# Optimization experiments

Measured on AMD Instinct MI355X. Metric: run time of the kernel, lower is better.

Reference implementation:

```python
import jax, jax.numpy as jnp
import numpy as np

NUM_HEAD = 16
HEAD_DIM = 64
SEQ, BATCH, DMODEL = 2048, 2, 1024


def setup_inputs() -> dict:
    key = jax.random.key(0)
    ks = jax.random.split(key, 6)
    xavier = lambda k, shp: jax.random.uniform(
        k, shp, jnp.float32, -1.0, 1.0) * np.sqrt(6.0 / (shp[0] + shp[1]))
    query = jax.random.normal(ks[0], (SEQ, BATCH, DMODEL), jnp.float32)
    q_w = xavier(ks[1], (DMODEL, DMODEL))
    k_w = xavier(ks[2], (DMODEL, DMODEL))
    v_w = xavier(ks[3], (DMODEL, DMODEL))
    out_w = xavier(ks[4], (DMODEL, DMODEL))
    zeros = jnp.zeros((DMODEL,), jnp.float32)
    # causal mask: True = masked out (key position after query position)
    causal = jnp.triu(jnp.ones((SEQ, SEQ), bool), k=1)
    attn_mask = jnp.broadcast_to(causal, (BATCH, SEQ, SEQ))
    return {
        "query": query,
        "q_w": q_w, "q_b": zeros,
        "k_w": k_w, "k_b": zeros,
        "v_w": v_w, "v_b": zeros,
        "out_w": out_w, "out_b": zeros,
        "attn_mask": attn_mask,
    }


def reference(query, q_w, q_b, k_w, k_b, v_w, v_b, out_w, out_b, attn_mask):
    S, B, _ = query.shape
    H, Dh = NUM_HEAD, HEAD_DIM
    scale = 1.0 / np.sqrt(Dh)
    # self-attention: key = value = query
    q = (query @ q_w.T + q_b).reshape(S, B, H, Dh)
    k = (query @ k_w.T + k_b).reshape(S, B, H, Dh)
    v = (query @ v_w.T + v_b).reshape(S, B, H, Dh)
    # scores: [B, H, S(query), S(key)]
    scores = jnp.einsum('sbhd,tbhd->bhst', q, k) * scale
    scores = jnp.where(attn_mask[:, None, :, :], -jnp.inf, scores)
    attn = jax.nn.softmax(scores, axis=-1)
    # context: [S, B, H, Dh] -> [S, B, H*Dh]
    ctx = jnp.einsum('bhst,tbhd->sbhd', attn, v).reshape(S, B, H * Dh)
    return ctx @ out_w.T + out_b
```

## Files before the change

kernel.cpp:

```cpp
#include <hip/hip_runtime.h>
#include <hip/hip_bf16.h>

typedef __bf16 bf16;
typedef __attribute__((ext_vector_type(2))) __bf16 bf16x2;
typedef __attribute__((ext_vector_type(4))) __bf16 bf16x4;
typedef __attribute__((ext_vector_type(8))) __bf16 bf16x8;
typedef __attribute__((ext_vector_type(4))) float f32x4;

static_assert(sizeof(bf16x8) == 16, "bf16x8 must be 16B");

#define S_LEN 2048
#define BATCH_N 2
#define DM 1024
#define NHEAD 16
#define HDIM 64
#define LOG2E 1.44269504088896f

__device__ __forceinline__ void async_cp16(const void* g, void* l) {
    __builtin_amdgcn_global_load_lds(
        (const __attribute__((address_space(1))) void*)g,
        (__attribute__((address_space(3))) void*)l, 16, 0, 0);
}

__global__ __launch_bounds__(256)
void cvt_all(const float* __restrict__ q,
             const float* __restrict__ w0, const float* __restrict__ w1,
             const float* __restrict__ w2, const float* __restrict__ w3,
             bf16* __restrict__ Xb,
             bf16* __restrict__ W0, bf16* __restrict__ W1,
             bf16* __restrict__ W2, bf16* __restrict__ W3) {
    const int blk = blockIdx.x;
    const float* src;
    bf16* dst;
    size_t base;
    if (blk < 2048) {
        src = q; dst = Xb; base = (size_t)blk * 2048;
    } else {
        const int w = (blk - 2048) >> 9;
        const int r = (blk - 2048) & 511;
        base = (size_t)r * 2048;
        src = (w == 0) ? w0 : (w == 1) ? w1 : (w == 2) ? w2 : w3;
        dst = (w == 0) ? W0 : (w == 1) ? W1 : (w == 2) ? W2 : W3;
    }
    const size_t i = base + (size_t)threadIdx.x * 8;
    const f32x4 a = *(const f32x4*)(src + i);
    const f32x4 b = *(const f32x4*)(src + i + 4);
    bf16x8 r8;
    r8[0] = (bf16)a[0]; r8[1] = (bf16)a[1]; r8[2] = (bf16)a[2]; r8[3] = (bf16)a[3];
    r8[4] = (bf16)b[0]; r8[5] = (bf16)b[1]; r8[6] = (bf16)b[2]; r8[7] = (bf16)b[3];
    *(bf16x8*)(dst + i) = r8;
}

__device__ __forceinline__ void gemm_tile(const bf16* __restrict__ A,
                                          const bf16* __restrict__ W,
                                          int row0, int col0, int Kdim,
                                          f32x4 acc[4][4]) {
    __shared__ bf16 As[128 * 32];
    __shared__ bf16 Bs[128 * 32];
    const int tid  = threadIdx.x;
    const int lane = tid & 63;
    const int wv   = tid >> 6;
    const int wr = wv >> 1, wc = wv & 1;
    const int qr = lane & 15, quad = lane >> 4;

    const int srow = wv * 16 + (lane >> 2);
    const int scol = (lane & 3) * 8;
    const bf16* Ap = A + (size_t)(row0 + srow) * Kdim + scol;
    const bf16* Wp = W + (size_t)(col0 + srow) * Kdim + scol;
    bf16* lA0 = As + wv * 512;
    bf16* lA1 = As + 64 * 32 + wv * 512;
    bf16* lB0 = Bs + wv * 512;
    bf16* lB1 = Bs + 64 * 32 + wv * 512;

    const f32x4 fzero = {0.f, 0.f, 0.f, 0.f};
    #pragma unroll
    for (int mi = 0; mi < 4; ++mi)
        #pragma unroll
        for (int ni = 0; ni < 4; ++ni)
            acc[mi][ni] = fzero;

    for (int k0 = 0; k0 < Kdim; k0 += 32) {
        __syncthreads();
        async_cp16(Ap + k0, lA0);
        async_cp16(Ap + (size_t)64 * Kdim + k0, lA1);
        async_cp16(Wp + k0, lB0);
        async_cp16(Wp + (size_t)64 * Kdim + k0, lB1);
        __syncthreads();

        bf16x8 af[4], bfr[4];
        #pragma unroll
        for (int mi = 0; mi < 4; ++mi)
            af[mi] = *(const bf16x8*)(As + (wr * 64 + mi * 16 + qr) * 32 + quad * 8);
        #pragma unroll
        for (int ni = 0; ni < 4; ++ni)
            bfr[ni] = *(const bf16x8*)(Bs + (wc * 64 + ni * 16 + qr) * 32 + quad * 8);
        #pragma unroll
        for (int mi = 0; mi < 4; ++mi)
            #pragma unroll
            for (int ni = 0; ni < 4; ++ni)
                acc[mi][ni] = __builtin_amdgcn_mfma_f32_16x16x32_bf16(
                    af[mi], bfr[ni], acc[mi][ni], 0, 0, 0);
    }
}

__global__ __launch_bounds__(256)
void qkv_kernel(const bf16* __restrict__ X,
                const bf16* __restrict__ Wq, const float* __restrict__ bq,
                const bf16* __restrict__ Wk, const float* __restrict__ bk,
                const bf16* __restrict__ Wv, const float* __restrict__ bv,
                bf16* __restrict__ Q, bf16* __restrict__ Kt, bf16* __restrict__ Vt) {
    const int mat  = blockIdx.z;
    const bf16*  W    = (mat == 0) ? Wq : (mat == 1) ? Wk : Wv;
    const float* bias = (mat == 0) ? bq : (mat == 1) ? bk : bv;
    const int col0 = blockIdx.x * 128;
    const int row0 = blockIdx.y * 128;

    f32x4 acc[4][4];
    gemm_tile(X, W, row0, col0, DM, acc);

    const int lane = threadIdx.x & 63;
    const int wave = threadIdx.x >> 6;
    const int wr = wave >> 1, wc = wave & 1;
    const int qr = lane & 15, quad = lane >> 4;

    #pragma unroll
    for (int ni = 0; ni < 4; ++ni) {
        const int n  = col0 + wc * 64 + ni * 16 + qr;
        const float bn = bias[n];
        const int h = n >> 6, dh = n & 63;
        #pragma unroll
        for (int mi = 0; mi < 4; ++mi) {
            const int i0 = row0 + wr * 64 + mi * 16 + quad * 4;
            const float v0 = acc[mi][ni][0] + bn;
            const float v1 = acc[mi][ni][1] + bn;
            const float v2 = acc[mi][ni][2] + bn;
            const float v3 = acc[mi][ni][3] + bn;
            if (mat == 2) {
                const int s0 = i0 >> 1;
                bf16x2 e0 = {(bf16)v0, (bf16)v2};
                bf16x2 e1 = {(bf16)v1, (bf16)v3};
                *(bf16x2*)(Vt + ((size_t)h * HDIM + dh) * S_LEN + s0) = e0;
                *(bf16x2*)(Vt + ((size_t)(NHEAD + h) * HDIM + dh) * S_LEN + s0) = e1;
            } else {
                #pragma unroll
                for (int r = 0; r < 4; ++r) {
                    const int i = i0 + r;
                    const int s = i >> 1, b = i & 1;
                    const float v = (r == 0) ? v0 : (r == 1) ? v1 : (r == 2) ? v2 : v3;
                    if (mat == 0) {
                        Q[((size_t)(b * NHEAD + h) * S_LEN + s) * HDIM + dh] =
                            (bf16)(v * (0.125f * LOG2E));
                    } else {
                        Kt[((size_t)(b * NHEAD + h) * S_LEN + s) * HDIM + dh] = (bf16)v;
                    }
                }
            }
        }
    }
}

#define PLD 40
#define PT  640
#define RSTRIDE 36

#define MFMA(a, b, c) __builtin_amdgcn_mfma_f32_16x16x32_bf16(a, b, c, 0, 0, 0)
#define EX(x) __builtin_amdgcn_exp2f(x)

#define QK_TILE(j) \
    f32x4 sA##j = MFMA(k0, qlo##j, fzero); sA##j = MFMA(k1, qhi##j, sA##j); \
    f32x4 sB##j = MFMA(k2, qlo##j, fzero); sB##j = MFMA(k3, qhi##j, sB##j);

#define SFULL(j) do { \
    const float e0 = EX(sA##j[0]), e1 = EX(sA##j[1]), e2 = EX(sA##j[2]), e3 = EX(sA##j[3]); \
    const float f0 = EX(sB##j[0]), f1 = EX(sB##j[1]), f2 = EX(sB##j[2]), f3 = EX(sB##j[3]); \
    l##j += (e0 + e1 + e2 + e3) + (f0 + f1 + f2 + f3); \
    bf16x4 wa = {(bf16)e0, (bf16)e1, (bf16)e2, (bf16)e3}; \
    bf16x4 wb = {(bf16)f0, (bf16)f1, (bf16)f2, (bf16)f3}; \
    *(bf16x4*)(Pw + (j) * PT + qr * PLD + quad * 4)      = wa; \
    *(bf16x4*)(Pw + (j) * PT + qr * PLD + 16 + quad * 4) = wb; \
} while (0)

#define SMASK(j) do { \
    const int qrow = qb0 + 16 * (j) + qr; \
    const int ka = t * 32 + quad * 4; \
    const float e0 = (ka + 0  <= qrow) ? EX(sA##j[0]) : 0.f; \
    const float e1 = (ka + 1  <= qrow) ? EX(sA##j[1]) : 0.f; \
    const float e2 = (ka + 2  <= qrow) ? EX(sA##j[2]) : 0.f; \
    const float e3 = (ka + 3  <= qrow) ? EX(sA##j[3]) : 0.f; \
    const float f0 = (ka + 16 <= qrow) ? EX(sB##j[0]) : 0.f; \
    const float f1 = (ka + 17 <= qrow) ? EX(sB##j[1]) : 0.f; \
    const float f2 = (ka + 18 <= qrow) ? EX(sB##j[2]) : 0.f; \
    const float f3 = (ka + 19 <= qrow) ? EX(sB##j[3]) : 0.f; \
    l##j += (e0 + e1 + e2 + e3) + (f0 + f1 + f2 + f3); \
    bf16x4 wa = {(bf16)e0, (bf16)e1, (bf16)e2, (bf16)e3}; \
    bf16x4 wb = {(bf16)f0, (bf16)f1, (bf16)f2, (bf16)f3}; \
    *(bf16x4*)(Pw + (j) * PT + qr * PLD + quad * 4)      = wa; \
    *(bf16x4*)(Pw + (j) * PT + qr * PLD + 16 + quad * 4) = wb; \
} while (0)

__global__ __launch_bounds__(256)
void attn_part(const bf16* __restrict__ Q, const bf16* __restrict__ K,
               const bf16* __restrict__ Vt,
               bf16* __restrict__ Pout, float* __restrict__ Pl) {
    __shared__ __align__(16) char smem[27648];
    const int lane = threadIdx.x & 63;
    const int wave = threadIdx.x >> 6;
    const int qr = lane & 15, quad = lane >> 4;
    const int bh = blockIdx.y;
    const int f  = blockIdx.x;
    int qb, c;
    if (f < 8)       { qb = f;                c = 0; }
    else if (f < 24) { qb = 8 + ((f - 8) >> 1);  c = (f - 8) & 1; }
    else if (f < 48) { qb = 16 + (f - 24) / 3;   c = (f - 24) % 3; }
    else             { qb = 24 + ((f - 48) >> 2); c = (f - 48) & 3; }
    const int qb0    = qb * 64;
    const int tdiag  = qb * 2;
    const int ntiles = 2 * qb + 2;
    const int t0     = c * 16;
    const int tend   = min(t0 + 16, ntiles);

    const bf16* Qb = Q  + (size_t)bh * S_LEN * HDIM;
    const bf16* Kb = K  + (size_t)bh * S_LEN * HDIM;
    const bf16* Vb = Vt + (size_t)bh * HDIM * S_LEN;

    const bf16x8 qlo0 = *(const bf16x8*)(Qb + (size_t)(qb0 + qr) * HDIM + quad * 8);
    const bf16x8 qhi0 = *(const bf16x8*)(Qb + (size_t)(qb0 + qr) * HDIM + quad * 8 + 32);
    const bf16x8 qlo1 = *(const bf16x8*)(Qb + (size_t)(qb0 + 16 + qr) * HDIM + quad * 8);
    const bf16x8 qhi1 = *(const bf16x8*)(Qb + (size_t)(qb0 + 16 + qr) * HDIM + quad * 8 + 32);
    const bf16x8 qlo2 = *(const bf16x8*)(Qb + (size_t)(qb0 + 32 + qr) * HDIM + quad * 8);
    const bf16x8 qhi2 = *(const bf16x8*)(Qb + (size_t)(qb0 + 32 + qr) * HDIM + quad * 8 + 32);
    const bf16x8 qlo3 = *(const bf16x8*)(Qb + (size_t)(qb0 + 48 + qr) * HDIM + quad * 8);
    const bf16x8 qhi3 = *(const bf16x8*)(Qb + (size_t)(qb0 + 48 + qr) * HDIM + quad * 8 + 32);

    const f32x4 fzero = {0.f, 0.f, 0.f, 0.f};
    f32x4 o0_0 = fzero, o0_1 = fzero, o0_2 = fzero, o0_3 = fzero;
    f32x4 o1_0 = fzero, o1_1 = fzero, o1_2 = fzero, o1_3 = fzero;
    f32x4 o2_0 = fzero, o2_1 = fzero, o2_2 = fzero, o2_3 = fzero;
    f32x4 o3_0 = fzero, o3_1 = fzero, o3_2 = fzero, o3_3 = fzero;
    float l0 = 0.f, l1 = 0.f, l2 = 0.f, l3 = 0.f;
    bf16* Pw = (bf16*)smem + wave * (4 * PT);

    for (int t = t0 + wave; t < tend; t += 4) {
        const bf16* kp = Kb + ((size_t)t * 32 + qr) * HDIM + quad * 8;
        const bf16x8 k0 = *(const bf16x8*)(kp);
        const bf16x8 k1 = *(const bf16x8*)(kp + 32);
        const bf16x8 k2 = *(const bf16x8*)(kp + 16 * HDIM);
        const bf16x8 k3 = *(const bf16x8*)(kp + 16 * HDIM + 32);
        const bf16* vp = Vb + (size_t)qr * S_LEN + t * 32 + quad * 8;
        const bf16x8 v0 = *(const bf16x8*)(vp);
        const bf16x8 v1 = *(const bf16x8*)(vp + 16 * S_LEN);
        const bf16x8 v2 = *(const bf16x8*)(vp + 32 * S_LEN);
        const bf16x8 v3 = *(const bf16x8*)(vp + 48 * S_LEN);

        if (t < tdiag) {
            QK_TILE(0); SFULL(0);
            QK_TILE(1); SFULL(1);
            QK_TILE(2); SFULL(2);
            QK_TILE(3); SFULL(3);
        } else {
            QK_TILE(0); SMASK(0);
            QK_TILE(1); SMASK(1);
            QK_TILE(2); SMASK(2);
            QK_TILE(3); SMASK(3);
        }

        const bf16x8 pf0 = *(const bf16x8*)(Pw + 0 * PT + qr * PLD + quad * 8);
        const bf16x8 pf1 = *(const bf16x8*)(Pw + 1 * PT + qr * PLD + quad * 8);
        const bf16x8 pf2 = *(const bf16x8*)(Pw + 2 * PT + qr * PLD + quad * 8);
        const bf16x8 pf3 = *(const bf16x8*)(Pw + 3 * PT + qr * PLD + quad * 8);
        o0_0 = MFMA(v0, pf0, o0_0); o0_1 = MFMA(v1, pf0, o0_1);
        o0_2 = MFMA(v2, pf0, o0_2); o0_3 = MFMA(v3, pf0, o0_3);
        o1_0 = MFMA(v0, pf1, o1_0); o1_1 = MFMA(v1, pf1, o1_1);
        o1_2 = MFMA(v2, pf1, o1_2); o1_3 = MFMA(v3, pf1, o1_3);
        o2_0 = MFMA(v0, pf2, o2_0); o2_1 = MFMA(v1, pf2, o2_1);
        o2_2 = MFMA(v2, pf2, o2_2); o2_3 = MFMA(v3, pf2, o2_3);
        o3_0 = MFMA(v0, pf3, o3_0); o3_1 = MFMA(v1, pf3, o3_1);
        o3_2 = MFMA(v2, pf3, o3_2); o3_3 = MFMA(v3, pf3, o3_3);
    }

    __syncthreads();
    float* red = (float*)smem;
    if (wave != 0) {
        float* rp = red + ((size_t)(wave - 1) * 64 + lane) * RSTRIDE;
        *(f32x4*)(rp +  0) = o0_0; *(f32x4*)(rp +  4) = o0_1;
        *(f32x4*)(rp +  8) = o0_2; *(f32x4*)(rp + 12) = o0_3;
        *(f32x4*)(rp + 16) = o1_0; *(f32x4*)(rp + 20) = o1_1;
        *(f32x4*)(rp + 24) = o1_2; *(f32x4*)(rp + 28) = o1_3;
        rp[32] = l0; rp[33] = l1;
    }
    __syncthreads();
    if (wave == 0) {
        #pragma unroll
        for (int w = 0; w < 3; ++w) {
            const float* rp = red + ((size_t)w * 64 + lane) * RSTRIDE;
            o0_0 += *(const f32x4*)(rp +  0); o0_1 += *(const f32x4*)(rp +  4);
            o0_2 += *(const f32x4*)(rp +  8); o0_3 += *(const f32x4*)(rp + 12);
            o1_0 += *(const f32x4*)(rp + 16); o1_1 += *(const f32x4*)(rp + 20);
            o1_2 += *(const f32x4*)(rp + 24); o1_3 += *(const f32x4*)(rp + 28);
            l0 += rp[32]; l1 += rp[33];
        }
    }
    __syncthreads();
    if (wave != 0) {
        float* rp = red + ((size_t)(wave - 1) * 64 + lane) * RSTRIDE;
        *(f32x4*)(rp +  0) = o2_0; *(f32x4*)(rp +  4) = o2_1;
        *(f32x4*)(rp +  8) = o2_2; *(f32x4*)(rp + 12) = o2_3;
        *(f32x4*)(rp + 16) = o3_0; *(f32x4*)(rp + 20) = o3_1;
        *(f32x4*)(rp + 24) = o3_2; *(f32x4*)(rp + 28) = o3_3;
        rp[32] = l2; rp[33] = l3;
    }
    __syncthreads();
    if (wave == 0) {
        #pragma unroll
        for (int w = 0; w < 3; ++w) {
            const float* rp = red + ((size_t)w * 64 + lane) * RSTRIDE;
            o2_0 += *(const f32x4*)(rp +  0); o2_1 += *(const f32x4*)(rp +  4);
            o2_2 += *(const f32x4*)(rp +  8); o2_3 += *(const f32x4*)(rp + 12);
            o3_0 += *(const f32x4*)(rp + 16); o3_1 += *(const f32x4*)(rp + 20);
            o3_2 += *(const f32x4*)(rp + 24); o3_3 += *(const f32x4*)(rp + 28);
            l2 += rp[32]; l3 += rp[33];
        }
        l0 += __shfl_xor(l0, 16); l0 += __shfl_xor(l0, 32);
        l1 += __shfl_xor(l1, 16); l1 += __shfl_xor(l1, 32);
        l2 += __shfl_xor(l2, 16); l2 += __shfl_xor(l2, 32);
        l3 += __shfl_xor(l3, 16); l3 += __shfl_xor(l3, 32);

        const size_t sidx = ((size_t)bh * 32 + qb) * 4 + c;
        bf16* po = Pout + sidx * 4096;
        float* pl = Pl + sidx * 64;
        #define PWRITE(ov, ni_, jrow_) do { \
            bf16x4 cc = {(bf16)ov[0], (bf16)ov[1], (bf16)ov[2], (bf16)ov[3]}; \
            *(bf16x4*)(po + (size_t)((jrow_) * 16 + qr) * 64 + (ni_) * 16 + quad * 4) = cc; \
        } while (0)
        PWRITE(o0_0, 0, 0); PWRITE(o0_1, 1, 0); PWRITE(o0_2, 2, 0); PWRITE(o0_3, 3, 0);
        PWRITE(o1_0, 0, 1); PWRITE(o1_1, 1, 1); PWRITE(o1_2, 2, 1); PWRITE(o1_3, 3, 1);
        PWRITE(o2_0, 0, 2); PWRITE(o2_1, 1, 2); PWRITE(o2_2, 2, 2); PWRITE(o2_3, 3, 2);
        PWRITE(o3_0, 0, 3); PWRITE(o3_1, 1, 3); PWRITE(o3_2, 2, 3); PWRITE(o3_3, 3, 3);
        #undef PWRITE
        if (quad == 0) {
            pl[qr]      = l0;
            pl[16 + qr] = l1;
            pl[32 + qr] = l2;
            pl[48 + qr] = l3;
        }
    }
}

__global__ __launch_bounds__(256)
void attn_reduce(const bf16* __restrict__ Pout, const float* __restrict__ Pl,
                 bf16* __restrict__ ctx) {
    const int qb = blockIdx.x, bh = blockIdx.y;
    const int b = bh >> 4, h = bh & 15;
    const int nc = (qb < 8) ? 1 : (qb < 16) ? 2 : (qb < 24) ? 3 : 4;
    const int tid = threadIdx.x;
    const int row = tid >> 2;
    const int dg  = (tid & 3) * 16;
    const size_t base = ((size_t)bh * 32 + qb) * 4;

    float acc[16];
    #pragma unroll
    for (int i = 0; i < 16; ++i) acc[i] = 0.f;
    float lsum = 0.f;
    for (int cc = 0; cc < nc; ++cc) {
        const bf16* po = Pout + (base + cc) * 4096 + (size_t)row * 64 + dg;
        const bf16x8 x0 = *(const bf16x8*)(po);
        const bf16x8 x1 = *(const bf16x8*)(po + 8);
        #pragma unroll
        for (int i = 0; i < 8; ++i) { acc[i] += (float)x0[i]; acc[8 + i] += (float)x1[i]; }
        lsum += Pl[(base + cc) * 64 + row];
    }
    const float inv = 1.f / lsum;
    bf16x8 y0, y1;
    #pragma unroll
    for (int i = 0; i < 8; ++i) { y0[i] = (bf16)(acc[i] * inv); y1[i] = (bf16)(acc[8 + i] * inv); }
    bf16* cp = ctx + ((size_t)(qb * 64 + row) * BATCH_N + b) * DM + h * 64 + dg;
    *(bf16x8*)cp = y0;
    *(bf16x8*)(cp + 8) = y1;
}

__global__ __launch_bounds__(256)
void proj_kernel(const bf16* __restrict__ X, const bf16* __restrict__ W,
                 const float* __restrict__ bias, float* __restrict__ out) {
    const int col0 = blockIdx.x * 128;
    const int row0 = blockIdx.y * 128;
    f32x4 acc[4][4];
    gemm_tile(X, W, row0, col0, DM, acc);

    const int lane = threadIdx.x & 63;
    const int wave = threadIdx.x >> 6;
    const int wr = wave >> 1, wc = wave & 1;
    const int qr = lane & 15, quad = lane >> 4;

    #pragma unroll
    for (int ni = 0; ni < 4; ++ni) {
        const int n = col0 + wc * 64 + ni * 16 + qr;
        const float bn = bias[n];
        #pragma unroll
        for (int mi = 0; mi < 4; ++mi) {
            #pragma unroll
            for (int r = 0; r < 4; ++r) {
                const int i = row0 + wr * 64 + mi * 16 + quad * 4 + r;
                out[(size_t)i * DM + n] = acc[mi][ni][r] + bn;
            }
        }
    }
}

extern "C" void kernel_launch(void* const* d_in, const int* in_sizes, int n_in,
                              void* d_out, int out_size, void* d_ws, size_t ws_size,
                              hipStream_t stream) {
    (void)in_sizes; (void)n_in; (void)out_size; (void)ws_size;
    const float* query = (const float*)d_in[0];
    const float* q_w   = (const float*)d_in[1];
    const float* q_b   = (const float*)d_in[2];
    const float* k_w   = (const float*)d_in[3];
    const float* k_b   = (const float*)d_in[4];
    const float* v_w   = (const float*)d_in[5];
    const float* v_b   = (const float*)d_in[6];
    const float* out_w = (const float*)d_in[7];
    const float* out_b = (const float*)d_in[8];

    char* ws = (char*)d_ws;
    bf16*  Qb   = (bf16*)(ws);
    bf16*  Kb   = (bf16*)(ws + ((size_t)8  << 20));
    bf16*  Vt   = (bf16*)(ws + ((size_t)16 << 20));
    bf16*  ctx  = (bf16*)(ws + ((size_t)24 << 20));
    bf16*  Wob  = (bf16*)(ws + ((size_t)32 << 20));
    bf16*  Xb   = (bf16*)(ws + ((size_t)34 << 20));
    bf16*  Wqb  = (bf16*)(ws + ((size_t)42 << 20));
    bf16*  Wkb  = (bf16*)(ws + ((size_t)44 << 20));
    bf16*  Wvb  = (bf16*)(ws + ((size_t)46 << 20));
    bf16*  Pout = (bf16*)(ws + ((size_t)34 << 20));
    float* Pl   = (float*)(ws + ((size_t)66 << 20));
    float* out  = (float*)d_out;

    dim3 blk(256);
    cvt_all<<<dim3(2048 + 4 * 512), blk, 0, stream>>>(
        query, q_w, k_w, v_w, out_w, Xb, Wqb, Wkb, Wvb, Wob);

    qkv_kernel<<<dim3(DM / 128, (S_LEN * BATCH_N) / 128, 3), blk, 0, stream>>>(
        Xb, Wqb, q_b, Wkb, k_b, Wvb, v_b, Qb, Kb, Vt);
    attn_part<<<dim3(80, BATCH_N * NHEAD), blk, 0, stream>>>(Qb, Kb, Vt, Pout, Pl);
    attn_reduce<<<dim3(S_LEN / 64, BATCH_N * NHEAD), blk, 0, stream>>>(Pout, Pl, ctx);
    proj_kernel<<<dim3(DM / 128, (S_LEN * BATCH_N) / 128), blk, 0, stream>>>(
        ctx, Wob, out_b, out);
}
```

Baseline: 232.9 us.

## Fuse attention partial reduce into attn_part with paired causal q-blocks

Each attention block now handles two query blocks, qb and 31-qb, one after the other and covers the full key range for each. It normalizes the output in-kernel and writes ctx directly. This removes the separate attn_reduce kernel and the bf16 partial-output round trip through global memory. The cost is far fewer blocks (512 instead of 2560) with longer serial loops per wave, so there is less parallelism and latency hiding. Shared memory also grows because the P buffer no longer overlaps the reduction area.

```diff
diff --git a/kernel.cpp b/kernel.cpp
--- a/kernel.cpp
+++ b/kernel.cpp
@@ -200,182 +200,145 @@
 
 __global__ __launch_bounds__(256)
 void attn_part(const bf16* __restrict__ Q, const bf16* __restrict__ K,
-               const bf16* __restrict__ Vt,
-               bf16* __restrict__ Pout, float* __restrict__ Pl) {
-    __shared__ __align__(16) char smem[27648];
+               const bf16* __restrict__ Vt, bf16* __restrict__ ctx) {
+    __shared__ __align__(16) char smem[27648 + 20480];
     const int lane = threadIdx.x & 63;
     const int wave = threadIdx.x >> 6;
     const int qr = lane & 15, quad = lane >> 4;
     const int bh = blockIdx.y;
-    const int f  = blockIdx.x;
-    int qb, c;
-    if (f < 8)       { qb = f;                c = 0; }
-    else if (f < 24) { qb = 8 + ((f - 8) >> 1);  c = (f - 8) & 1; }
-    else if (f < 48) { qb = 16 + (f - 24) / 3;   c = (f - 24) % 3; }
-    else             { qb = 24 + ((f - 48) >> 2); c = (f - 48) & 3; }
-    const int qb0    = qb * 64;
-    const int tdiag  = qb * 2;
-    const int ntiles = 2 * qb + 2;
-    const int t0     = c * 16;
-    const int tend   = min(t0 + 16, ntiles);
+    const int b = bh >> 4, h = bh & 15;
 
     const bf16* Qb = Q  + (size_t)bh * S_LEN * HDIM;
     const bf16* Kb = K  + (size_t)bh * S_LEN * HDIM;
     const bf16* Vb = Vt + (size_t)bh * HDIM * S_LEN;
-
-    const bf16x8 qlo0 = *(const bf16x8*)(Qb + (size_t)(qb0 + qr) * HDIM + quad * 8);
-    const bf16x8 qhi0 = *(const bf16x8*)(Qb + (size_t)(qb0 + qr) * HDIM + quad * 8 + 32);
-    const bf16x8 qlo1 = *(const bf16x8*)(Qb + (size_t)(qb0 + 16 + qr) * HDIM + quad * 8);
-    const bf16x8 qhi1 = *(const bf16x8*)(Qb + (size_t)(qb0 + 16 + qr) * HDIM + quad * 8 + 32);
-    const bf16x8 qlo2 = *(const bf16x8*)(Qb + (size_t)(qb0 + 32 + qr) * HDIM + quad * 8);
-    const bf16x8 qhi2 = *(const bf16x8*)(Qb + (size_t)(qb0 + 32 + qr) * HDIM + quad * 8 + 32);
-    const bf16x8 qlo3 = *(const bf16x8*)(Qb + (size_t)(qb0 + 48 + qr) * HDIM + quad * 8);
-    const bf16x8 qhi3 = *(const bf16x8*)(Qb + (size_t)(qb0 + 48 + qr) * HDIM + quad * 8 + 32);
-
+    float* red = (float*)smem;
+    bf16* Pw = (bf16*)(smem + 27648) + wave * (4 * PT);
     const f32x4 fzero = {0.f, 0.f, 0.f, 0.f};
-    f32x4 o0_0 = fzero, o0_1 = fzero, o0_2 = fzero, o0_3 = fzero;
-    f32x4 o1_0 = fzero, o1_1 = fzero, o1_2 = fzero, o1_3 = fzero;
-    f32x4 o2_0 = fzero, o2_1 = fzero, o2_2 = fzero, o2_3 = fzero;
-    f32x4 o3_0 = fzero, o3_1 = fzero, o3_2 = fzero, o3_3 = fzero;
-    float l0 = 0.f, l1 = 0.f, l2 = 0.f, l3 = 0.f;
-    bf16* Pw = (bf16*)smem + wave * (4 * PT);
-
-    for (int t = t0 + wave; t < tend; t += 4) {
-        const bf16* kp = Kb + ((size_t)t * 32 + qr) * HDIM + quad * 8;
-        const bf16x8 k0 = *(const bf16x8*)(kp);
-        const bf16x8 k1 = *(const bf16x8*)(kp + 32);
-        const bf16x8 k2 = *(const bf16x8*)(kp + 16 * HDIM);
-        const bf16x8 k3 = *(const bf16x8*)(kp + 16 * HDIM + 32);
-        const bf16* vp = Vb + (size_t)qr * S_LEN + t * 32 + quad * 8;
-        const bf16x8 v0 = *(const bf16x8*)(vp);
-        const bf16x8 v1 = *(const bf16x8*)(vp + 16 * S_LEN);
-        const bf16x8 v2 = *(const bf16x8*)(vp + 32 * S_LEN);
-        const bf16x8 v3 = *(const bf16x8*)(vp + 48 * S_LEN);
-
-        if (t < tdiag) {
-            QK_TILE(0); SFULL(0);
-            QK_TILE(1); SFULL(1);
-            QK_TILE(2); SFULL(2);
-            QK_TILE(3); SFULL(3);
-        } else {
-            QK_TILE(0); SMASK(0);
-            QK_TILE(1); SMASK(1);
-            QK_TILE(2); SMASK(2);
-            QK_TILE(3); SMASK(3);
-        }
-
-        const bf16x8 pf0 = *(const bf16x8*)(Pw + 0 * PT + qr * PLD + quad * 8);
-        const bf16x8 pf1 = *(const bf16x8*)(Pw + 1 * PT + qr * PLD + quad * 8);
-        const bf16x8 pf2 = *(const bf16x8*)(Pw + 2 * PT + qr * PLD + quad * 8);
-        const bf16x8 pf3 = *(const bf16x8*)(Pw + 3 * PT + qr * PLD + quad * 8);
-        o0_0 = MFMA(v0, pf0, o0_0); o0_1 = MFMA(v1, pf0, o0_1);
-        o0_2 = MFMA(v2, pf0, o0_2); o0_3 = MFMA(v3, pf0, o0_3);
-        o1_0 = MFMA(v0, pf1, o1_0); o1_1 = MFMA(v1, pf1, o1_1);
-        o1_2 = MFMA(v2, pf1, o1_2); o1_3 = MFMA(v3, pf1, o1_3);
-        o2_0 = MFMA(v0, pf2, o2_0); o2_1 = MFMA(v1, pf2, o2_1);
-        o2_2 = MFMA(v2, pf2, o2_2); o2_3 = MFMA(v3, pf2, o2_3);
-        o3_0 = MFMA(v0, pf3, o3_0); o3_1 = MFMA(v1, pf3, o3_1);
-        o3_2 = MFMA(v2, pf3, o3_2); o3_3 = MFMA(v3, pf3, o3_3);
+
+    for (int phase = 0; phase < 2; ++phase) {
+        const int qb = phase ? (31 - (int)blockIdx.x) : (int)blockIdx.x;
+        const int qb0    = qb * 64;
+        const int tdiag  = qb * 2;
+        const int ntiles = 2 * qb + 2;
+
+        const bf16x8 qlo0 = *(const bf16x8*)(Qb + (size_t)(qb0 + qr) * HDIM + quad * 8);
+        const bf16x8 qhi0 = *(const bf16x8*)(Qb + (size_t)(qb0 + qr) * HDIM + quad * 8 + 32);
+        const bf16x8 qlo1 = *(const bf16x8*)(Qb + (size_t)(qb0 + 16 + qr) * HDIM + quad * 8);
+        const bf16x8 qhi1 = *(const bf16x8*)(Qb + (size_t)(qb0 + 16 + qr) * HDIM + quad * 8 + 32);
+        const bf16x8 qlo2 = *(const bf16x8*)(Qb + (size_t)(qb0 + 32 + qr) * HDIM + quad * 8);
+        const bf16x8 qhi2 = *(const bf16x8*)(Qb + (size_t)(qb0 + 32 + qr) * HDIM + quad * 8 + 32);
+        const bf16x8 qlo3 = *(const bf16x8*)(Qb + (size_t)(qb0 + 48 + qr) * HDIM + quad * 8);
+        const bf16x8 qhi3 = *(const bf16x8*)(Qb + (size_t)(qb0 + 48 + qr) * HDIM + quad * 8 + 32);
+
+        f32x4 o0_0 = fzero, o0_1 = fzero, o0_2 = fzero, o0_3 = fzero;
+        f32x4 o1_0 = fzero, o1_1 = fzero, o1_2 = fzero, o1_3 = fzero;
+        f32x4 o2_0 = fzero, o2_1 = fzero, o2_2 = fzero, o2_3 = fzero;
+        f32x4 o3_0 = fzero, o3_1 = fzero, o3_2 = fzero, o3_3 = fzero;
+        float l0 = 0.f, l1 = 0.f, l2 = 0.f, l3 = 0.f;
+
+        for (int t = wave; t < ntiles; t += 4) {
+            const bf16* kp = Kb + ((size_t)t * 32 + qr) * HDIM + quad * 8;
+            const bf16x8 k0 = *(const bf16x8*)(kp);
+            const bf16x8 k1 = *(const bf16x8*)(kp + 32);
+            const bf16x8 k2 = *(const bf16x8*)(kp + 16 * HDIM);
+            const bf16x8 k3 = *(const bf16x8*)(kp + 16 * HDIM + 32);
+            const bf16* vp = Vb + (size_t)qr * S_LEN + t * 32 + quad * 8;
+            const bf16x8 v0 = *(const bf16x8*)(vp);
+            const bf16x8 v1 = *(const bf16x8*)(vp + 16 * S_LEN);
+            const bf16x8 v2 = *(const bf16x8*)(vp + 32 * S_LEN);
+            const bf16x8 v3 = *(const bf16x8*)(vp + 48 * S_LEN);
+
+            if (t < tdiag) {
+                QK_TILE(0); SFULL(0);
+                QK_TILE(1); SFULL(1);
+                QK_TILE(2); SFULL(2);
+                QK_TILE(3); SFULL(3);
+            } else {
+                QK_TILE(0); SMASK(0);
+                QK_TILE(1); SMASK(1);
+                QK_TILE(2); SMASK(2);
+                QK_TILE(3); SMASK(3);
+            }
+
+            const bf16x8 pf0 = *(const bf16x8*)(Pw + 0 * PT + qr * PLD + quad * 8);
+            const bf16x8 pf1 = *(const bf16x8*)(Pw + 1 * PT + qr * PLD + quad * 8);
+            const bf16x8 pf2 = *(const bf16x8*)(Pw + 2 * PT + qr * PLD + quad * 8);
+            const bf16x8 pf3 = *(const bf16x8*)(Pw + 3 * PT + qr * PLD + quad * 8);
+            o0_0 = MFMA(v0, pf0, o0_0); o0_1 = MFMA(v1, pf0, o0_1);
+            o0_2 = MFMA(v2, pf0, o0_2); o0_3 = MFMA(v3, pf0, o0_3);
+            o1_0 = MFMA(v0, pf1, o1_0); o1_1 = MFMA(v1, pf1, o1_1);
+            o1_2 = MFMA(v2, pf1, o1_2); o1_3 = MFMA(v3, pf1, o1_3);
+            o2_0 = MFMA(v0, pf2, o2_0); o2_1 = MFMA(v1, pf2, o2_1);
+            o2_2 = MFMA(v2, pf2, o2_2); o2_3 = MFMA(v3, pf2, o2_3);
+            o3_0 = MFMA(v0, pf3, o3_0); o3_1 = MFMA(v1, pf3, o3_1);
+            o3_2 = MFMA(v2, pf3, o3_2); o3_3 = MFMA(v3, pf3, o3_3);
+        }
+
+        __syncthreads();
+        if (wave != 0) {
+            float* rp = red + ((size_t)(wave - 1) * 64 + lane) * RSTRIDE;
+            *(f32x4*)(rp +  0) = o0_0; *(f32x4*)(rp +  4) = o0_1;
+            *(f32x4*)(rp +  8) = o0_2; *(f32x4*)(rp + 12) = o0_3;
+            *(f32x4*)(rp + 16) = o1_0; *(f32x4*)(rp + 20) = o1_1;
+            *(f32x4*)(rp + 24) = o1_2; *(f32x4*)(rp + 28) = o1_3;
+            rp[32] = l0; rp[33] = l1;
+        }
+        __syncthreads();
+        if (wave == 0) {
+            #pragma unroll
+            for (int w = 0; w < 3; ++w) {
+                const float* rp = red + ((size_t)w * 64 + lane) * RSTRIDE;
+                o0_0 += *(const f32x4*)(rp +  0); o0_1 += *(const f32x4*)(rp +  4);
+                o0_2 += *(const f32x4*)(rp +  8); o0_3 += *(const f32x4*)(rp + 12);
+                o1_0 += *(const f32x4*)(rp + 16); o1_1 += *(const f32x4*)(rp + 20);
+                o1_2 += *(const f32x4*)(rp + 24); o1_3 += *(const f32x4*)(rp + 28);
+                l0 += rp[32]; l1 += rp[33];
+            }
+        }
+        __syncthreads();
+        if (wave != 0) {
+            float* rp = red + ((size_t)(wave - 1) * 64 + lane) * RSTRIDE;
+            *(f32x4*)(rp +  0) = o2_0; *(f32x4*)(rp +  4) = o2_1;
+            *(f32x4*)(rp +  8) = o2_2; *(f32x4*)(rp + 12) = o2_3;
+            *(f32x4*)(rp + 16) = o3_0; *(f32x4*)(rp + 20) = o3_1;
+            *(f32x4*)(rp + 24) = o3_2; *(f32x4*)(rp + 28) = o3_3;
+            rp[32] = l2; rp[33] = l3;
+        }
+        __syncthreads();
+        if (wave == 0) {
+            #pragma unroll
+            for (int w = 0; w < 3; ++w) {
+                const float* rp = red + ((size_t)w * 64 + lane) * RSTRIDE;
+                o2_0 += *(const f32x4*)(rp +  0); o2_1 += *(const f32x4*)(rp +  4);
+                o2_2 += *(const f32x4*)(rp +  8); o2_3 += *(const f32x4*)(rp + 12);
+                o3_0 += *(const f32x4*)(rp + 16); o3_1 += *(const f32x4*)(rp + 20);
+                o3_2 += *(const f32x4*)(rp + 24); o3_3 += *(const f32x4*)(rp + 28);
+                l2 += rp[32]; l3 += rp[33];
+            }
+            l0 += __shfl_xor(l0, 16); l0 += __shfl_xor(l0, 32);
+            l1 += __shfl_xor(l1, 16); l1 += __shfl_xor(l1, 32);
+            l2 += __shfl_xor(l2, 16); l2 += __shfl_xor(l2, 32);
+            l3 += __shfl_xor(l3, 16); l3 += __shfl_xor(l3, 32);
+            const float n0 = 1.f / l0, n1 = 1.f / l1, n2 = 1.f / l2, n3 = 1.f / l3;
+
+            #define CWRITE(ov, ni_, jrow_, nf_) do { \
+                bf16x4 cc = {(bf16)(ov[0] * (nf_)), (bf16)(ov[1] * (nf_)), \
+                             (bf16)(ov[2] * (nf_)), (bf16)(ov[3] * (nf_))}; \
+                const int s_ = qb0 + (jrow_) * 16 + qr; \
+                *(bf16x4*)(ctx + ((size_t)s_ * BATCH_N + b) * DM \
+                           + h * HDIM + (ni_) * 16 + quad * 4) = cc; \
+            } while (0)
+            CWRITE(o0_0, 0, 0, n0); CWRITE(o0_1, 1, 0, n0);
+            CWRITE(o0_2, 2, 0, n0); CWRITE(o0_3, 3, 0, n0);
+            CWRITE(o1_0, 0, 1, n1); CWRITE(o1_1, 1, 1, n1);
+            CWRITE(o1_2, 2, 1, n1); CWRITE(o1_3, 3, 1, n1);
+            CWRITE(o2_0, 0, 2, n2); CWRITE(o2_1, 1, 2, n2);
+            CWRITE(o2_2, 2, 2, n2); CWRITE(o2_3, 3, 2, n2);
+            CWRITE(o3_0, 0, 3, n3); CWRITE(o3_1, 1, 3, n3);
+            CWRITE(o3_2, 2, 3, n3); CWRITE(o3_3, 3, 3, n3);
+            #undef CWRITE
+        }
     }
-
-    __syncthreads();
-    float* red = (float*)smem;
-    if (wave != 0) {
-        float* rp = red + ((size_t)(wave - 1) * 64 + lane) * RSTRIDE;
-        *(f32x4*)(rp +  0) = o0_0; *(f32x4*)(rp +  4) = o0_1;
-        *(f32x4*)(rp +  8) = o0_2; *(f32x4*)(rp + 12) = o0_3;
-        *(f32x4*)(rp + 16) = o1_0; *(f32x4*)(rp + 20) = o1_1;
-        *(f32x4*)(rp + 24) = o1_2; *(f32x4*)(rp + 28) = o1_3;
-        rp[32] = l0; rp[33] = l1;
-    }
-    __syncthreads();
-    if (wave == 0) {
-        #pragma unroll
-        for (int w = 0; w < 3; ++w) {
-            const float* rp = red + ((size_t)w * 64 + lane) * RSTRIDE;
-            o0_0 += *(const f32x4*)(rp +  0); o0_1 += *(const f32x4*)(rp +  4);
-            o0_2 += *(const f32x4*)(rp +  8); o0_3 += *(const f32x4*)(rp + 12);
-            o1_0 += *(const f32x4*)(rp + 16); o1_1 += *(const f32x4*)(rp + 20);
-            o1_2 += *(const f32x4*)(rp + 24); o1_3 += *(const f32x4*)(rp + 28);
-            l0 += rp[32]; l1 += rp[33];
-        }
-    }
-    __syncthreads();
-    if (wave != 0) {
-        float* rp = red + ((size_t)(wave - 1) * 64 + lane) * RSTRIDE;
-        *(f32x4*)(rp +  0) = o2_0; *(f32x4*)(rp +  4) = o2_1;
-        *(f32x4*)(rp +  8) = o2_2; *(f32x4*)(rp + 12) = o2_3;
-        *(f32x4*)(rp + 16) = o3_0; *(f32x4*)(rp + 20) = o3_1;
-        *(f32x4*)(rp + 24) = o3_2; *(f32x4*)(rp + 28) = o3_3;
-        rp[32] = l2; rp[33] = l3;
-    }
-    __syncthreads();
-    if (wave == 0) {
-        #pragma unroll
-        for (int w = 0; w < 3; ++w) {
-            const float* rp = red + ((size_t)w * 64 + lane) * RSTRIDE;
-            o2_0 += *(const f32x4*)(rp +  0); o2_1 += *(const f32x4*)(rp +  4);
-            o2_2 += *(const f32x4*)(rp +  8); o2_3 += *(const f32x4*)(rp + 12);
-            o3_0 += *(const f32x4*)(rp + 16); o3_1 += *(const f32x4*)(rp + 20);
-            o3_2 += *(const f32x4*)(rp + 24); o3_3 += *(const f32x4*)(rp + 28);
-            l2 += rp[32]; l3 += rp[33];
-        }
-        l0 += __shfl_xor(l0, 16); l0 += __shfl_xor(l0, 32);
-        l1 += __shfl_xor(l1, 16); l1 += __shfl_xor(l1, 32);
-        l2 += __shfl_xor(l2, 16); l2 += __shfl_xor(l2, 32);
-        l3 += __shfl_xor(l3, 16); l3 += __shfl_xor(l3, 32);
-
-        const size_t sidx = ((size_t)bh * 32 + qb) * 4 + c;
-        bf16* po = Pout + sidx * 4096;
-        float* pl = Pl + sidx * 64;
-        #define PWRITE(ov, ni_, jrow_) do { \
-            bf16x4 cc = {(bf16)ov[0], (bf16)ov[1], (bf16)ov[2], (bf16)ov[3]}; \
-            *(bf16x4*)(po + (size_t)((jrow_) * 16 + qr) * 64 + (ni_) * 16 + quad * 4) = cc; \
-        } while (0)
-        PWRITE(o0_0, 0, 0); PWRITE(o0_1, 1, 0); PWRITE(o0_2, 2, 0); PWRITE(o0_3, 3, 0);
-        PWRITE(o1_0, 0, 1); PWRITE(o1_1, 1, 1); PWRITE(o1_2, 2, 1); PWRITE(o1_3, 3, 1);
-        PWRITE(o2_0, 0, 2); PWRITE(o2_1, 1, 2); PWRITE(o2_2, 2, 2); PWRITE(o2_3, 3, 2);
-        PWRITE(o3_0, 0, 3); PWRITE(o3_1, 1, 3); PWRITE(o3_2, 2, 3); PWRITE(o3_3, 3, 3);
-        #undef PWRITE
-        if (quad == 0) {
-            pl[qr]      = l0;
-            pl[16 + qr] = l1;
-            pl[32 + qr] = l2;
-            pl[48 + qr] = l3;
-        }
-    }
-}
-
-__global__ __launch_bounds__(256)
-void attn_reduce(const bf16* __restrict__ Pout, const float* __restrict__ Pl,
-                 bf16* __restrict__ ctx) {
-    const int qb = blockIdx.x, bh = blockIdx.y;
-    const int b = bh >> 4, h = bh & 15;
-    const int nc = (qb < 8) ? 1 : (qb < 16) ? 2 : (qb < 24) ? 3 : 4;
-    const int tid = threadIdx.x;
-    const int row = tid >> 2;
-    const int dg  = (tid & 3) * 16;
-    const size_t base = ((size_t)bh * 32 + qb) * 4;
-
-    float acc[16];
-    #pragma unroll
-    for (int i = 0; i < 16; ++i) acc[i] = 0.f;
-    float lsum = 0.f;
-    for (int cc = 0; cc < nc; ++cc) {
-        const bf16* po = Pout + (base + cc) * 4096 + (size_t)row * 64 + dg;
-        const bf16x8 x0 = *(const bf16x8*)(po);
-        const bf16x8 x1 = *(const bf16x8*)(po + 8);
-        #pragma unroll
-        for (int i = 0; i < 8; ++i) { acc[i] += (float)x0[i]; acc[8 + i] += (float)x1[i]; }
-        lsum += Pl[(base + cc) * 64 + row];
-    }
-    const float inv = 1.f / lsum;
-    bf16x8 y0, y1;
-    #pragma unroll
-    for (int i = 0; i < 8; ++i) { y0[i] = (bf16)(acc[i] * inv); y1[i] = (bf16)(acc[8 + i] * inv); }
-    bf16* cp = ctx + ((size_t)(qb * 64 + row) * BATCH_N + b) * DM + h * 64 + dg;
-    *(bf16x8*)cp = y0;
-    *(bf16x8*)(cp + 8) = y1;
 }
 
 __global__ __launch_bounds__(256)
@@ -430,8 +393,6 @@
     bf16*  Wqb  = (bf16*)(ws + ((size_t)42 << 20));
     bf16*  Wkb  = (bf16*)(ws + ((size_t)44 << 20));
     bf16*  Wvb  = (bf16*)(ws + ((size_t)46 << 20));
-    bf16*  Pout = (bf16*)(ws + ((size_t)34 << 20));
-    float* Pl   = (float*)(ws + ((size_t)66 << 20));
     float* out  = (float*)d_out;
 
     dim3 blk(256);
@@ -440,8 +401,7 @@
 
     qkv_kernel<<<dim3(DM / 128, (S_LEN * BATCH_N) / 128, 3), blk, 0, stream>>>(
         Xb, Wqb, q_b, Wkb, k_b, Wvb, v_b, Qb, Kb, Vt);
-    attn_part<<<dim3(80, BATCH_N * NHEAD), blk, 0, stream>>>(Qb, Kb, Vt, Pout, Pl);
-    attn_reduce<<<dim3(S_LEN / 64, BATCH_N * NHEAD), blk, 0, stream>>>(Pout, Pl, ctx);
+    attn_part<<<dim3(16, BATCH_N * NHEAD), blk, 0, stream>>>(Qb, Kb, Vt, ctx);
     proj_kernel<<<dim3(DM / 128, (S_LEN * BATCH_N) / 128), blk, 0, stream>>>(
         ctx, Wob, out_b, out);
 }
```

Result: faster. 219.1 us (-5.9%).
